# Optimization experiments

Hardware: AMD Instinct MI355X
Metric: run time of the kernel (lower is better)

The kernel has to match this reference:

```python
import jax, jax.numpy as jnp
import numpy as np

HEADS = 16
DK = 64
THETA = 10000.0


def _rope(x, cos, sin):
    # x: (B, S, H, dk) -> rotate consecutive pairs as complex numbers
    xr = x.reshape(*x.shape[:-1], -1, 2)
    a, b = xr[..., 0], xr[..., 1]
    c = cos[None, :, None, :]  # (1, S, 1, dk//2)
    s = sin[None, :, None, :]
    out = jnp.stack([a * c - b * s, a * s + b * c], axis=-1)
    return out.reshape(x.shape)


def setup_inputs() -> dict:
    key = jax.random.key(0)
    ks = jax.random.split(key, 5)
    B, S, D = 4, 2048, 1024
    x = jax.random.normal(ks[0], (B, S, D), dtype=jnp.float32)
    scale = 1.0 / np.sqrt(D).astype(np.float32)
    Wq = jax.random.normal(ks[1], (D, D), dtype=jnp.float32) * scale
    Wk = jax.random.normal(ks[2], (D, D), dtype=jnp.float32) * scale
    Wv = jax.random.normal(ks[3], (D, D), dtype=jnp.float32) * scale
    Wo = jax.random.normal(ks[4], (D, D), dtype=jnp.float32) * scale
    # freqs_cis = exp(i * t * theta^{-2j/dk}), represented as cos/sin
    t = jnp.arange(S, dtype=jnp.float32)
    inv_freq = 1.0 / (THETA ** (jnp.arange(0, DK, 2, dtype=jnp.float32) / DK))
    ang = t[:, None] * inv_freq[None, :]  # (S, dk//2)
    return {"in_features": x, "freqs_cos": jnp.cos(ang), "freqs_sin": jnp.sin(ang),
            "Wq": Wq, "Wk": Wk, "Wv": Wv, "Wo": Wo}


def reference(in_features, freqs_cos, freqs_sin, Wq, Wk, Wv, Wo):
    B, S, D = in_features.shape
    H = HEADS
    dk = D // H
    # Linear projections (torch Linear: x @ W.T)
    q = (in_features @ Wq.T).reshape(B, S, H, dk)
    k = (in_features @ Wk.T).reshape(B, S, H, dk)
    v = (in_features @ Wv.T).reshape(B, S, H, dk)
    q = _rope(q, freqs_cos, freqs_sin)
    k = _rope(k, freqs_cos, freqs_sin)
    scale = 1.0 / jnp.sqrt(jnp.asarray(dk, dtype=q.dtype))
    scores = jnp.einsum("bqhd,bkhd->bhqk", q, k) * scale
    mask = jnp.tril(jnp.ones((S, S), dtype=bool))
    scores = jnp.where(mask[None, None, :, :], scores, -jnp.inf)
    attn = jax.nn.softmax(scores, axis=-1)
    out = jnp.einsum("bhqk,bkhd->bqhd", attn, v).reshape(B, S, D)
    return out @ Wo.T
```

## Files before the change

kernel.cpp:

```cpp
#include <hip/hip_runtime.h>
#include <hip/hip_bf16.h>

typedef __attribute__((ext_vector_type(8))) __bf16 bf16x8;
typedef __attribute__((ext_vector_type(4))) __bf16 bf16x4;
typedef __attribute__((ext_vector_type(4))) float f32x4;
typedef __attribute__((ext_vector_type(2))) unsigned int u32x2;

static __device__ __forceinline__ f32x4 mfma_bf16(bf16x8 a, bf16x8 b, f32x4 c) {
  return __builtin_amdgcn_mfma_f32_16x16x32_bf16(a, b, c, 0, 0, 0);
}

static __device__ __forceinline__ void gload_lds16(const void* g, void* l) {
  __builtin_amdgcn_global_load_lds(
      (__attribute__((address_space(1))) unsigned int*)g,
      (__attribute__((address_space(3))) unsigned int*)l, 16, 0, 0);
}

static __device__ __forceinline__ unsigned int cvt_pk_bf16(float lo, float hi) {
  unsigned int r;
  asm volatile("v_cvt_pk_bf16_f32 %0, %1, %2" : "=v"(r) : "v"(lo), "v"(hi));
  return r;
}

__global__ void cvt_bf16(const float* __restrict__ in, __bf16* __restrict__ out, int n4) {
  int i = blockIdx.x * blockDim.x + threadIdx.x;
  if (i >= n4) return;
  f32x4 v = ((const f32x4*)in)[i];
  bf16x4 o;
#pragma unroll
  for (int k = 0; k < 4; ++k) o[k] = (__bf16)v[k];
  ((bf16x4*)out)[i] = o;
}

__global__ void cvt_w4(const float* __restrict__ w0, const float* __restrict__ w1,
                       const float* __restrict__ w2, const float* __restrict__ w3,
                       __bf16* __restrict__ o0, __bf16* __restrict__ o1,
                       __bf16* __restrict__ o2, __bf16* __restrict__ o3) {
  const float* in; __bf16* out;
  switch (blockIdx.y) {
    case 0: in = w0; out = o0; break;
    case 1: in = w1; out = o1; break;
    case 2: in = w2; out = o2; break;
    default: in = w3; out = o3; break;
  }
  int i = blockIdx.x * blockDim.x + threadIdx.x;
  f32x4 v = ((const f32x4*)in)[i];
  bf16x4 o;
#pragma unroll
  for (int k = 0; k < 4; ++k) o[k] = (__bf16)v[k];
  ((bf16x4*)out)[i] = o;
}

#define ISSUE_A(kt, slot)                                                   \
  {                                                                         \
    const int k0 = (kt) * 64;                                               \
    __bf16* d = Al + (slot) * 16384 + t * 8;                                \
    gload_lds16(Ag + k0, d);                                                \
    gload_lds16(Ag + (size_t)64 * K + k0, d + 4096);                        \
    gload_lds16(Ag + (size_t)128 * K + k0, d + 8192);                       \
    gload_lds16(Ag + (size_t)192 * K + k0, d + 12288);                      \
  }
#define ISSUE_B(kt, slot)                                                   \
  {                                                                         \
    const int k0 = (kt) * 64;                                               \
    __bf16* d = Bl + (slot) * 8192 + t * 8;                                 \
    gload_lds16(Wg + k0, d);                                                \
    gload_lds16(Wg + (size_t)64 * K + k0, d + 4096);                        \
  }

#define GEMM_PIPELINE                                                       \
  constexpr int K = 1024;                                                   \
  constexpr int NT = K / 64;                                                \
  extern __shared__ __align__(16) __bf16 dynlds[];                          \
  __bf16* Al = dynlds;                                                      \
  __bf16* Bl = dynlds + 49152;                                              \
  const int t = threadIdx.x;                                                \
  const int lane = t & 63, wave = t >> 6;                                   \
  const int g = lane >> 4, ln = lane & 15;                                  \
  const int wm = wave >> 1, wn = wave & 1;                                  \
  f32x4 acc[4][4] = {};                                                     \
  const int srow8 = t >> 3;                                                 \
  const int scole = (((t & 7) ^ ((t >> 3) & 7)) << 3);                      \
  const __bf16* Ag = A + (size_t)(bm * 256 + srow8) * K + scole;            \
  const __bf16* Wg = W + (size_t)(bn * 128 + srow8) * K + scole;            \
  const int axr = ln & 7;                                                   \
  int aoff[4], boff[4];                                                     \
  _Pragma("unroll") for (int i = 0; i < 4; ++i)                             \
    aoff[i] = (wm * 64 + i * 16 + ln) * 64;                                 \
  _Pragma("unroll") for (int j = 0; j < 4; ++j)                             \
    boff[j] = (wn * 64 + j * 16 + ln) * 64;                                 \
  ISSUE_B(0, 0); ISSUE_A(0, 0); ISSUE_A(1, 1);                              \
  asm volatile("s_waitcnt vmcnt(4)" ::: "memory");                          \
  __builtin_amdgcn_s_barrier();                                             \
  int sa = 0;                                                               \
  for (int tt = 0; tt < NT; ++tt) {                                         \
    const __bf16* Ab = Al + sa * 16384;                                     \
    const __bf16* Bb = Bl + (tt & 1) * 8192;                                \
    bf16x8 af[4], bf[4];                                                    \
    _Pragma("unroll") for (int i = 0; i < 4; ++i)                           \
      af[i] = *(const bf16x8*)(Ab + aoff[i] + ((g ^ axr) << 3));            \
    _Pragma("unroll") for (int j = 0; j < 4; ++j)                           \
      bf[j] = *(const bf16x8*)(Bb + boff[j] + ((g ^ axr) << 3));            \
    if (tt + 1 < NT) ISSUE_B(tt + 1, (tt + 1) & 1);                         \
    if (tt + 2 < NT) ISSUE_A(tt + 2, sa == 0 ? 2 : sa - 1);                 \
    __builtin_amdgcn_s_barrier();                                           \
    asm volatile("s_waitcnt lgkmcnt(0)" ::: "memory");                      \
    __builtin_amdgcn_sched_barrier(0);                                      \
    __builtin_amdgcn_s_setprio(1);                                          \
    _Pragma("unroll") for (int i = 0; i < 4; ++i)                           \
      _Pragma("unroll") for (int j = 0; j < 4; ++j)                         \
        acc[i][j] = mfma_bf16(af[i], bf[j], acc[i][j]);                     \
    __builtin_amdgcn_s_setprio(0);                                          \
    __builtin_amdgcn_s_barrier();                                           \
    _Pragma("unroll") for (int i = 0; i < 4; ++i)                           \
      af[i] = *(const bf16x8*)(Ab + aoff[i] + (((4 | g) ^ axr) << 3));      \
    _Pragma("unroll") for (int j = 0; j < 4; ++j)                           \
      bf[j] = *(const bf16x8*)(Bb + boff[j] + (((4 | g) ^ axr) << 3));      \
    if (tt < NT - 2) { asm volatile("s_waitcnt vmcnt(4)" ::: "memory"); }   \
    else             { asm volatile("s_waitcnt vmcnt(0)" ::: "memory"); }   \
    __builtin_amdgcn_s_barrier();                                           \
    asm volatile("s_waitcnt lgkmcnt(0)" ::: "memory");                      \
    __builtin_amdgcn_sched_barrier(0);                                      \
    __builtin_amdgcn_s_setprio(1);                                          \
    _Pragma("unroll") for (int i = 0; i < 4; ++i)                           \
      _Pragma("unroll") for (int j = 0; j < 4; ++j)                         \
        acc[i][j] = mfma_bf16(af[i], bf[j], acc[i][j]);                     \
    __builtin_amdgcn_s_setprio(0);                                          \
    __builtin_amdgcn_s_barrier();                                           \
    sa = (sa == 2) ? 0 : sa + 1;                                            \
  }

template <int MODE>
__global__ __launch_bounds__(512, 1)
void gemm256(const __bf16* __restrict__ A, const __bf16* __restrict__ W,
             void* __restrict__ outp,
             const float* __restrict__ fcos, const float* __restrict__ fsin) {
  const int lin = blockIdx.x + blockIdx.y * 8;
  const int bm = (lin & 7) + 8 * ((lin >> 3) & 3);
  const int bn = lin >> 5;

  GEMM_PIPELINE

#pragma unroll
  for (int i = 0; i < 4; ++i) {
    const int mbase = bm * 256 + wm * 64 + i * 16 + g * 4;
#pragma unroll
    for (int j = 0; j < 4; ++j) {
      const int col = bn * 128 + wn * 64 + j * 16 + ln;
      if constexpr (MODE == 0 || MODE == 1) {
        const int fi = (col & 63) >> 1;
        const bool odd = (col & 1) != 0;
        __bf16* O = (__bf16*)outp;
#pragma unroll
        for (int r = 0; r < 4; ++r) {
          const int row = mbase + r;
          const int tok = row & 2047;
          const float cs = fcos[tok * 32 + fi];
          const float sn = fsin[tok * 32 + fi];
          const float own = acc[i][j][r];
          const float oth = __shfl_xor(own, 1);
          float val = own * cs + (odd ? oth * sn : -oth * sn);
          if constexpr (MODE == 0) val *= 0.1803368802f;
          O[(size_t)row * 1024 + col] = (__bf16)val;
        }
      } else if constexpr (MODE == 2) {
        __bf16* O = (__bf16*)outp;
        const int bb = mbase >> 11;
        const int tok = mbase & 2047;
        bf16x4 pk;
#pragma unroll
        for (int r = 0; r < 4; ++r) pk[r] = (__bf16)acc[i][j][r];
        *(bf16x4*)(O + ((size_t)(bb * 1024 + col)) * 2048 + tok) = pk;
      } else {
        float* O = (float*)outp;
#pragma unroll
        for (int r = 0; r < 4; ++r)
          O[(size_t)(mbase + r) * 1024 + col] = acc[i][j][r];
      }
    }
  }
}

static __device__ __forceinline__ void sm_pack_pv(
    f32x4* sa, float& m, float& l, f32x4* o,
    unsigned int* Pw, const __bf16* Vb, const int g, const int ln) {
  const float a0 = fmaxf(fmaxf(sa[0][0], sa[0][1]), sa[0][2]);
  const float a1 = fmaxf(fmaxf(sa[0][3], sa[1][0]), sa[1][1]);
  const float a2 = fmaxf(fmaxf(sa[1][2], sa[1][3]), sa[2][0]);
  const float a3 = fmaxf(fmaxf(sa[2][1], sa[2][2]), sa[2][3]);
  const float a4 = fmaxf(fmaxf(sa[3][0], sa[3][1]), sa[3][2]);
  float pm = fmaxf(fmaxf(fmaxf(a0, a1), a2), fmaxf(fmaxf(a3, a4), sa[3][3]));

  if (__any(pm > m + 8.f)) {
    pm = fmaxf(pm, __shfl_xor(pm, 16));
    pm = fmaxf(pm, __shfl_xor(pm, 32));
    const float mn = fmaxf(m, pm);
    const float alpha = exp2f(m - mn);
    m = mn;
    l *= alpha;
#pragma unroll
    for (int c2 = 0; c2 < 4; ++c2)
#pragma unroll
      for (int r = 0; r < 4; ++r) o[c2][r] *= alpha;
  }

  float p[4][4];
#pragma unroll
  for (int c = 0; c < 4; ++c)
#pragma unroll
    for (int r = 0; r < 4; ++r) p[c][r] = exp2f(sa[c][r] - m);

  float ts[8];
#pragma unroll
  for (int i = 0; i < 8; ++i) ts[i] = p[i >> 2][i & 3] + p[2 + (i >> 2)][i & 3];
#pragma unroll
  for (int st = 4; st >= 1; st >>= 1)
#pragma unroll
    for (int i = 0; i < st; ++i) ts[i] += ts[i + st];
  float rs = ts[0];
  rs += __shfl_xor(rs, 16);
  rs += __shfl_xor(rs, 32);
  l += rs;

  unsigned int* Pr = Pw + ln * 36;
#pragma unroll
  for (int c = 0; c < 4; ++c) {
    u32x2 w;
    w[0] = cvt_pk_bf16(p[c][0], p[c][1]);
    w[1] = cvt_pk_bf16(p[c][2], p[c][3]);
    *(u32x2*)(Pr + 8 * c + 2 * g) = w;
  }

  __builtin_amdgcn_s_setprio(1);
#pragma unroll
  for (int sh = 0; sh < 2; ++sh) {
    bf16x8 pb = *(const bf16x8*)((const __bf16*)Pw + ln * 72 + sh * 32 + g * 8);
#pragma unroll
    for (int c2 = 0; c2 < 4; ++c2) {
      bf16x8 vf = *(const bf16x8*)(Vb + sh * 2048 + (c2 * 16 + ln) * 32 + g * 8);
      o[c2] = mfma_bf16(vf, pb, o[c2]);
    }
  }
  __builtin_amdgcn_s_setprio(0);
}

__global__ __launch_bounds__(512, 6)
void attn_fwd(const __bf16* __restrict__ Q, const __bf16* __restrict__ Kk,
              const __bf16* __restrict__ Vt, __bf16* __restrict__ U) {
  constexpr int S = 2048;
  __shared__ __align__(16) __bf16 Klds[2][2 * 64 * 32];
  __shared__ __align__(16) __bf16 Vlds[2][2 * 64 * 32];
  __shared__ __align__(16) unsigned int Plds[8][16 * 36];

  const int t = threadIdx.x;
  const int lane = t & 63, wave = t >> 6;
  const int g = lane >> 4, ln = lane & 15;
  const int lin = blockIdx.x + blockIdx.y * 16;
  const int bh = (lin & 7) * 8 + ((lin >> 3) & 7);
  const int qt = 15 - (lin >> 6);
  const int b = bh >> 4, h = bh & 15;
  const int q0 = qt * 128;
  const int nt = 2 * qt + 2;

  const __bf16* Qb = Q + ((size_t)(b * S + q0 + wave * 16 + ln)) * 1024 + h * 64;
  bf16x8 qf0 = *(const bf16x8*)(Qb + g * 8);
  bf16x8 qf1 = *(const bf16x8*)(Qb + 32 + g * 8);

  f32x4 o[4] = {};
  float mrow = -3.0e38f, lrow = 0.f;

  const int half = t >> 8;
  const int srow = (t >> 2) & 63;
  const int scol = (t & 3) * 8;
  const __bf16* Kg = Kk + ((size_t)(b * S + srow)) * 1024 + h * 64 + half * 32 + scol;
  const __bf16* Vg = Vt + ((size_t)(b * 1024 + h * 64 + srow)) * 2048 + half * 32 + scol;

  gload_lds16(Kg, (__bf16*)Klds[0] + t * 8);
  gload_lds16(Vg, (__bf16*)Vlds[0] + t * 8);
  __syncthreads();

  for (int kt = 0; kt < nt; ++kt) {
    const int cur = kt & 1;
    if (kt + 1 < nt) {
      const size_t kv1 = (size_t)(kt + 1) * 64;
      gload_lds16(Kg + kv1 * 1024, (__bf16*)Klds[cur ^ 1] + t * 8);
      gload_lds16(Vg + kv1, (__bf16*)Vlds[cur ^ 1] + t * 8);
    }
    const int kv0 = kt * 64;

    f32x4 sa[4] = {};
    __builtin_amdgcn_s_setprio(1);
#pragma unroll
    for (int s = 0; s < 2; ++s) {
      const bf16x8 qf = s ? qf1 : qf0;
#pragma unroll
      for (int c = 0; c < 4; ++c) {
        bf16x8 kf = *(const bf16x8*)(Klds[cur] + s * 2048 + (c * 16 + ln) * 32 + g * 8);
        sa[c] = mfma_bf16(kf, qf, sa[c]);
      }
    }
    __builtin_amdgcn_s_setprio(0);

    const int rfbase = q0 + wave * 16;
    const int rq = rfbase + ln;
    if (kv0 + 63 > rfbase) {
#pragma unroll
      for (int c = 0; c < 4; ++c)
#pragma unroll
        for (int r = 0; r < 4; ++r)
          if (kv0 + c * 16 + g * 4 + r > rq) sa[c][r] = -1e30f;
    }

    sm_pack_pv(sa, mrow, lrow, o, Plds[wave], Vlds[cur], g, ln);
    __syncthreads();
  }

  const float rl = 1.0f / lrow;
  __bf16* Ub = U + ((size_t)(b * S + q0 + wave * 16 + ln)) * 1024 + h * 64;
#pragma unroll
  for (int c2 = 0; c2 < 4; ++c2) {
    bf16x4 pk4;
#pragma unroll
    for (int r = 0; r < 4; ++r) pk4[r] = (__bf16)(o[c2][r] * rl);
    *(bf16x4*)(Ub + 16 * c2 + 4 * g) = pk4;
  }
}

extern "C" void kernel_launch(void* const* d_in, const int* in_sizes, int n_in,
                              void* d_out, int out_size, void* d_ws, size_t ws_size,
                              hipStream_t stream) {
  const float* x    = (const float*)d_in[0];
  const float* fcos = (const float*)d_in[1];
  const float* fsin = (const float*)d_in[2];
  const float* Wq   = (const float*)d_in[3];
  const float* Wk   = (const float*)d_in[4];
  const float* Wv   = (const float*)d_in[5];
  const float* Wo   = (const float*)d_in[6];

  char* ws = (char*)d_ws;
  __bf16* xb  = (__bf16*)(ws);
  __bf16* Wqb = (__bf16*)(ws + (16u << 20));
  __bf16* Wkb = (__bf16*)(ws + (18u << 20));
  __bf16* Wvb = (__bf16*)(ws + (20u << 20));
  __bf16* Wob = (__bf16*)(ws + (22u << 20));
  __bf16* Qb  = (__bf16*)(ws + (24u << 20));
  __bf16* Kb  = (__bf16*)(ws + (40u << 20));
  __bf16* Vtb = (__bf16*)(ws + (56u << 20));
  __bf16* Ub  = xb;

  cvt_bf16<<<8192, 256, 0, stream>>>(x, xb, 8192 * 1024 / 4);
  cvt_w4<<<dim3(1024, 4), 256, 0, stream>>>(Wq, Wk, Wv, Wo, Wqb, Wkb, Wvb, Wob);

  dim3 gg(8, 32);
  const size_t lds = 131072;
  gemm256<0><<<gg, 512, lds, stream>>>(xb, Wqb, Qb,  fcos, fsin);
  gemm256<1><<<gg, 512, lds, stream>>>(xb, Wkb, Kb,  fcos, fsin);
  gemm256<2><<<gg, 512, lds, stream>>>(xb, Wvb, Vtb, nullptr, nullptr);
  attn_fwd<<<dim3(16, 64), 512, 0, stream>>>(Qb, Kb, Vtb, Ub);
  gemm256<3><<<gg, 512, lds, stream>>>(Ub, Wob, d_out, nullptr, nullptr);
}
```

Before: 187.2 us.

## Single-buffer K/V tiles through registers with padded LDS rows

Replaces the double-buffered direct global-to-LDS loads of K and V tiles with register prefetch of the next tile and a single padded (72-element stride) LDS buffer written after the current tile's compute. This shrinks LDS per block so more blocks can reside per CU, and launch bounds are raised to 8 blocks per CU accordingly. It adds an extra barrier per iteration and routes the loads through registers, which raises register pressure and may serialize the store against compute.

```diff
diff --git a/kernel.cpp b/kernel.cpp
--- a/kernel.cpp
+++ b/kernel.cpp
@@ -237,19 +237,19 @@
     bf16x8 pb = *(const bf16x8*)((const __bf16*)Pw + ln * 72 + sh * 32 + g * 8);
 #pragma unroll
     for (int c2 = 0; c2 < 4; ++c2) {
-      bf16x8 vf = *(const bf16x8*)(Vb + sh * 2048 + (c2 * 16 + ln) * 32 + g * 8);
+      bf16x8 vf = *(const bf16x8*)(Vb + (c2 * 16 + ln) * 72 + sh * 32 + g * 8);
       o[c2] = mfma_bf16(vf, pb, o[c2]);
     }
   }
   __builtin_amdgcn_s_setprio(0);
 }
 
-__global__ __launch_bounds__(512, 6)
+__global__ __launch_bounds__(512, 8)
 void attn_fwd(const __bf16* __restrict__ Q, const __bf16* __restrict__ Kk,
               const __bf16* __restrict__ Vt, __bf16* __restrict__ U) {
   constexpr int S = 2048;
-  __shared__ __align__(16) __bf16 Klds[2][2 * 64 * 32];
-  __shared__ __align__(16) __bf16 Vlds[2][2 * 64 * 32];
+  __shared__ __align__(16) __bf16 Klds[64 * 72];
+  __shared__ __align__(16) __bf16 Vlds[64 * 72];
   __shared__ __align__(16) unsigned int Plds[8][16 * 36];
 
   const int t = threadIdx.x;
@@ -269,22 +269,26 @@
   f32x4 o[4] = {};
   float mrow = -3.0e38f, lrow = 0.f;
 
-  const int half = t >> 8;
-  const int srow = (t >> 2) & 63;
-  const int scol = (t & 3) * 8;
-  const __bf16* Kg = Kk + ((size_t)(b * S + srow)) * 1024 + h * 64 + half * 32 + scol;
-  const __bf16* Vg = Vt + ((size_t)(b * 1024 + h * 64 + srow)) * 2048 + half * 32 + scol;
-
-  gload_lds16(Kg, (__bf16*)Klds[0] + t * 8);
-  gload_lds16(Vg, (__bf16*)Vlds[0] + t * 8);
+  const int srow = t >> 3;
+  const int schunk = (t & 7) * 8;
+  const __bf16* Kg = Kk + ((size_t)(b * S + srow)) * 1024 + h * 64 + schunk;
+  const __bf16* Vg = Vt + ((size_t)(b * 1024 + h * 64 + srow)) * 2048 + schunk;
+  __bf16* Kw = Klds + srow * 72 + schunk;
+  __bf16* Vw = Vlds + srow * 72 + schunk;
+
+  {
+    bf16x8 k0 = *(const bf16x8*)(Kg);
+    bf16x8 v0 = *(const bf16x8*)(Vg);
+    *(bf16x8*)Kw = k0;
+    *(bf16x8*)Vw = v0;
+  }
   __syncthreads();
 
   for (int kt = 0; kt < nt; ++kt) {
-    const int cur = kt & 1;
+    bf16x8 kreg, vreg;
     if (kt + 1 < nt) {
-      const size_t kv1 = (size_t)(kt + 1) * 64;
-      gload_lds16(Kg + kv1 * 1024, (__bf16*)Klds[cur ^ 1] + t * 8);
-      gload_lds16(Vg + kv1, (__bf16*)Vlds[cur ^ 1] + t * 8);
+      kreg = *(const bf16x8*)(Kg + (size_t)(kt + 1) * 64 * 1024);
+      vreg = *(const bf16x8*)(Vg + (kt + 1) * 64);
     }
     const int kv0 = kt * 64;
 
@@ -295,7 +299,7 @@
       const bf16x8 qf = s ? qf1 : qf0;
 #pragma unroll
       for (int c = 0; c < 4; ++c) {
-        bf16x8 kf = *(const bf16x8*)(Klds[cur] + s * 2048 + (c * 16 + ln) * 32 + g * 8);
+        bf16x8 kf = *(const bf16x8*)(Klds + (c * 16 + ln) * 72 + s * 32 + g * 8);
         sa[c] = mfma_bf16(kf, qf, sa[c]);
       }
     }
@@ -311,7 +315,13 @@
           if (kv0 + c * 16 + g * 4 + r > rq) sa[c][r] = -1e30f;
     }
 
-    sm_pack_pv(sa, mrow, lrow, o, Plds[wave], Vlds[cur], g, ln);
+    sm_pack_pv(sa, mrow, lrow, o, Plds[wave], Vlds, g, ln);
+
+    __syncthreads();
+    if (kt + 1 < nt) {
+      *(bf16x8*)Kw = kreg;
+      *(bf16x8*)Vw = vreg;
+    }
     __syncthreads();
   }
 
```

Measured after the change: 217.5 us. 16.2% more time.
